# Kernel optimization log

Measured on AMD Instinct MI355X. Metric: run time of the kernel, lower is better.

Reference implementation:

```python
import jax, jax.numpy as jnp
import numpy as np

K = 3  # spline order
G = 5  # grid_size

def bspline(x):
    # Cox-de Boor B-spline basis over uniform grid on [-1,1] extended by K knots each side.
    h = 2.0 / G
    grid = jnp.arange(-K, G + K + 1, dtype=x.dtype) * h - 1.0  # [G+2K+1]
    xe = x[..., None]
    b = ((xe >= grid[:-1]) & (xe < grid[1:])).astype(x.dtype)  # order-0 bases [..., G+2K]
    for p in range(1, K + 1):
        b = ((xe - grid[:-(p + 1)]) / (grid[p:-1] - grid[:-(p + 1)]) * b[..., :-1]
             + (grid[p + 1:] - xe) / (grid[p + 1:] - grid[1:-p]) * b[..., 1:])
    return b  # [..., G+K]

def kan_conv(x, wb, ws, k):
    # x: [B,Cin,H,W] -> patches [B, Cin*k*k, H', W'] -> KANLinear per spatial position
    p = jax.lax.conv_general_dilated_patches(x, (k, k), (1, 1), 'VALID')
    p = jnp.moveaxis(p, 1, -1)  # [B,H',W',F]
    base = jax.nn.silu(p) @ wb.T
    spline = jnp.einsum('bhwig,oig->bhwo', bspline(p), ws)
    return jnp.moveaxis(base + spline, -1, 1)  # [B,Cout,H',W']

def maxpool2(x):
    return jax.lax.reduce_window(x, -jnp.inf, jax.lax.max, (1, 1, 2, 2), (1, 1, 2, 2), 'VALID')

def setup_inputs() -> dict:
    key = jax.random.key(0)
    ks = jax.random.split(key, 9)
    B = 4096
    s = 0.1
    return {
        'x': jax.random.normal(ks[0], (B, 1, 28, 28), jnp.float32),
        'wb1': jax.random.normal(ks[1], (5, 9), jnp.float32) * s,
        'ws1': jax.random.normal(ks[2], (5, 9, G + K), jnp.float32) * s,
        'wb2': jax.random.normal(ks[3], (5, 125), jnp.float32) * s,
        'ws2': jax.random.normal(ks[4], (5, 125, G + K), jnp.float32) * s,
        'wb3': jax.random.normal(ks[5], (2, 45), jnp.float32) * s,
        'ws3': jax.random.normal(ks[6], (2, 45, G + K), jnp.float32) * s,
        'fc_w': jax.random.normal(ks[7], (200, 98), jnp.float32) * s,
        'fc_b': jnp.zeros((200,), jnp.float32),
    }

def reference(x, wb1, ws1, wb2, ws2, wb3, ws3, fc_w, fc_b):
    h = kan_conv(x, wb1, ws1, 3)    # [B,5,26,26]
    h = maxpool2(h)                 # [B,5,13,13]
    h = kan_conv(h, wb2, ws2, 5)    # [B,5,9,9]
    h = kan_conv(h, wb3, ws3, 3)    # [B,2,7,7]
    h = h.reshape(h.shape[0], -1)   # [B,98]
    return h @ fc_w.T + fc_b        # [B,200]
```

## Files before the change

kernel.cpp:

```cpp
#include <hip/hip_runtime.h>


typedef _Float16 h2 __attribute__((ext_vector_type(2)));
typedef _Float16 f16x8 __attribute__((ext_vector_type(8)));
typedef float f32x4 __attribute__((ext_vector_type(4)));
typedef unsigned int uint_t;
typedef unsigned long long u64;

__device__ __forceinline__ uint_t pk(float a, float b) {
    h2 v; v[0] = (_Float16)a; v[1] = (_Float16)b;
    union { h2 h; uint_t u; } c; c.h = v; return c.u;
}

__device__ __forceinline__ float silu_f(float v) {
    return v / (1.0f + __expf(-v));
}

struct RecW { u64 R0, R1; uint_t R2; };
__device__ __forceinline__ RecW rec_words(float v) {
    float s  = silu_f(v);
    float t  = (v + 2.2f) * 2.5f;
    float cf = floorf(t);
    int   c  = (int)cf;
    float u  = t - cf;
    float u2 = u * u, u3 = u2 * u;
    float w  = 1.0f - u;
    const float k6 = 0.16666667f;
    float n0 = k6 * u3;
    float n1 = k6 * (-3.0f * u3 + 3.0f * u2 + 3.0f * u + 1.0f);
    float n2 = k6 * (3.0f * u3 - 6.0f * u2 + 4.0f);
    float n3 = k6 * (w * w * w);
    u64 H = ((u64)pk(n1, n0) << 32) | (u64)pk(n3, n2);
    if ((unsigned)c > 10u) H = 0;
    int cc = c < 0 ? 0 : (c > 10 ? 10 : c);
    int L  = cc * 16 - 48;
    u64 sl_lo = (L < 64) ? (H << (L & 63)) : 0;
    u64 hi_a  = (L == 0) ? 0 : (H >> ((64 - L) & 63));
    u64 hi_b  = H << ((L - 64) & 63);
    u64 sl_hi = (L < 64) ? hi_a : hi_b;
    u64 sr    = H >> ((-L) & 63);
    u64 B0 = (L >= 0) ? sl_lo : sr;
    u64 B1 = (L >= 0) ? sl_hi : 0;
    RecW r;
    r.R0 = (B0 << 16) | (u64)pk(s, 0.0f);
    r.R1 = (B0 >> 48) | (B1 << 16);
    r.R2 = (uint_t)(B1 >> 48);
    return r;
}

__device__ __forceinline__ void write_rec16s(_Float16* p, int off, float v) {
    RecW rw = rec_words(v);
    uint4 lo, hi;
    lo.x = (uint_t)rw.R0; lo.y = (uint_t)(rw.R0 >> 32);
    lo.z = (uint_t)rw.R1; lo.w = (uint_t)(rw.R1 >> 32);
    hi.x = rw.R2; hi.y = 0; hi.z = 0; hi.w = 0;
    *(uint4*)(p + off)       = lo;
    *(uint4*)(p + (8 ^ off)) = hi;
}

__device__ __forceinline__ void write_rec10(_Float16* p, float v) {
    RecW rw = rec_words(v);
    uint_t* d = (uint_t*)p;
    d[0] = (uint_t)rw.R0; d[1] = (uint_t)(rw.R0 >> 32);
    d[2] = (uint_t)rw.R1; d[3] = (uint_t)(rw.R1 >> 32);
    d[4] = rw.R2;
}

#define FCWT_BYTE_OFF   0
#define W1COL_BYTE_OFF  78400
#define W2COL_BYTE_OFF  80320
#define W3COL_BYTE_OFF  99520

__global__ __launch_bounds__(256) void kan_prep(
    const float* __restrict__ wb1, const float* __restrict__ ws1,
    const float* __restrict__ wb2, const float* __restrict__ ws2,
    const float* __restrict__ wb3, const float* __restrict__ ws3,
    const float* __restrict__ fcw, float* __restrict__ fcwT,
    _Float16* __restrict__ w1col, _Float16* __restrict__ w2col,
    _Float16* __restrict__ w3col)
{
    int gtid = blockIdx.x * 256 + threadIdx.x;
    int gstr = gridDim.x * 256;
    for (int i = gtid; i < 19600; i += gstr) {
        int o = i / 98, j = i % 98;
        fcwT[j * 200 + o] = fcw[i];
    }
    for (int i = gtid; i < 960; i += gstr) {
        int n = i / 160, k = i % 160;
        int rec = k >> 4, f = k & 15;
        float v = 0.f;
        if (n < 5 && rec < 9 && f < 9)
            v = (f == 0) ? wb1[n * 9 + rec] : ws1[(n * 9 + rec) * 8 + (f - 1)];
        w1col[i] = (_Float16)v;
    }
    for (int i = gtid; i < 9600; i += gstr) {
        int n = i / 1600, k2 = i % 1600;
        int tap = k2 >> 6, k = k2 & 63;
        int di = tap / 5, dj = tap % 5;
        int c = k / 10, f = k % 10;
        float v = 0.f;
        if (n < 5 && k < 50 && f < 9) {
            int r = n * 125 + c * 25 + di * 5 + dj;
            v = (f == 0) ? wb2[r] : ws2[r * 8 + (f - 1)];
        }
        w2col[i] = (_Float16)v;
    }
    for (int i = gtid; i < 3456; i += gstr) {
        int n = i / 576, k2 = i % 576;
        int tap = k2 >> 6, k = k2 & 63;
        int di = tap / 3, dj = tap % 3;
        int c = k / 10, f = k % 10;
        float v = 0.f;
        if (n < 2 && k < 50 && f < 9) {
            int r = n * 45 + c * 9 + di * 3 + dj;
            v = (f == 0) ? wb3[r] : ws3[r * 8 + (f - 1)];
        }
        w3col[i] = (_Float16)v;
    }
}

__global__ __launch_bounds__(256) void kan_fused(
    const float* __restrict__ x,
    const _Float16* __restrict__ w1col,
    const _Float16* __restrict__ w2col,
    const _Float16* __restrict__ w3col,
    const float* __restrict__ fcwT,
    const float* __restrict__ fcb,
    float* __restrict__ out)
{
    __shared__ __align__(16) _Float16 smemA[12544];
    __shared__ __align__(16) float    smemB[504];
    float* buf = smemB;
    float* h3f = smemB + 405;

    const int b   = blockIdx.x;
    const int tid = threadIdx.x;
    const int wv  = __builtin_amdgcn_readfirstlane(tid >> 6);
    const int ln  = tid & 63;

    const int m   = ln & 15;
    const int kb  = ln >> 4;
    const int hr  = kb >> 1;
    const int s8  = (kb & 1) * 8;
    const int nn  = m < 5 ? m : 5;

#pragma unroll 1
    for (int i = tid; i < 784; i += 256)
        write_rec16s(&smemA[i * 16], (i & 4) << 1, x[b * 784 + i]);
    __syncthreads();

    {
        f16x8 Bf[5];
#pragma unroll
        for (int ks = 0; ks < 5; ++ks)
            Bf[ks] = *(const f16x8*)(w1col + nn * 160 + ks * 32 + kb * 8);
        const int dpix[10] = {0, 1, 2, 28, 29, 30, 56, 57, 58, 0};
#pragma unroll 1
        for (int tile = wv; tile < 43; tile += 4) {
            int p = tile * 16 + m; p = p > 675 ? 675 : p;
            int pix0 = (p / 26) * 28 + (p % 26);
            f32x4 acc = {0.f, 0.f, 0.f, 0.f};
#pragma unroll
            for (int ks = 0; ks < 5; ++ks) {
                int dp = hr ? dpix[2 * ks + 1] : dpix[2 * ks];
                int p2 = pix0 + dp;
                int addr = p2 * 16 + (s8 ^ ((p2 & 4) << 1));
                f16x8 av = *(const f16x8*)(smemA + addr);
                acc = __builtin_amdgcn_mfma_f32_16x16x32_f16(av, Bf[ks], acc, 0, 0, 0);
            }
            int srow = tile * 16 + kb * 4;
#pragma unroll
            for (int r = 0; r < 4; ++r) {
                int s = srow + r;
                if (m < 5 && s < 676)
                    smemA[s * 16 + (8 ^ ((s & 4) << 1)) + 2 + m] = (_Float16)acc[r];
            }
        }
    }
    __syncthreads();

    float mx0, mx1, mx2, mx3 = 0.f;
    {
        auto pool = [&](int i) -> float {
            int pp = i / 5, c = i % 5;
            int ph = pp / 13, pw = pp % 13;
            int s0 = ph * 52 + pw * 2;
            int s1 = s0 + 1, s2 = s0 + 26, s3 = s0 + 27;
            float v00 = (float)smemA[s0 * 16 + (8 ^ ((s0 & 4) << 1)) + 2 + c];
            float v01 = (float)smemA[s1 * 16 + (8 ^ ((s1 & 4) << 1)) + 2 + c];
            float v10 = (float)smemA[s2 * 16 + (8 ^ ((s2 & 4) << 1)) + 2 + c];
            float v11 = (float)smemA[s3 * 16 + (8 ^ ((s3 & 4) << 1)) + 2 + c];
            return fmaxf(fmaxf(v00, v01), fmaxf(v10, v11));
        };
        mx0 = pool(tid);
        mx1 = pool(tid + 256);
        mx2 = pool(tid + 512);
        if (tid < 77) mx3 = pool(tid + 768);
    }
    __syncthreads();

    {
        auto st = [&](int i, float v) {
            int pp = i / 5, c = i % 5;
            write_rec10(&smemA[pp * 72 + c * 10], v);
        };
        st(tid, mx0);
        st(tid + 256, mx1);
        st(tid + 512, mx2);
        if (tid < 77) st(tid + 768, mx3);
    }
    __syncthreads();

    {
        int p0 = wv * 16 + m;       p0 = p0 > 80 ? 80 : p0;
        int p1 = (wv + 4) * 16 + m; p1 = p1 > 80 ? 80 : p1;
        int ry0 = (p0 / 9) * 13 + (p0 % 9);
        int ry1 = (p1 / 9) * 13 + (p1 % 9);
        const bool two = (wv < 2);
        f32x4 acc0 = {0.f, 0.f, 0.f, 0.f}, acc1 = {0.f, 0.f, 0.f, 0.f};
#pragma unroll 1
        for (int tap = 0; tap < 25; ++tap) {
            int di = tap / 5, dj = tap % 5;
            const _Float16* wrow = w2col + nn * 1600 + tap * 64 + kb * 8;
            f16x8 bv0 = *(const f16x8*)(wrow);
            f16x8 bv1 = *(const f16x8*)(wrow + 32);
            int qoff = di * 13 + dj;
            const _Float16* ab0 = smemA + (ry0 + qoff) * 72 + kb * 8;
            acc0 = __builtin_amdgcn_mfma_f32_16x16x32_f16(*(const f16x8*)(ab0),      bv0, acc0, 0, 0, 0);
            acc0 = __builtin_amdgcn_mfma_f32_16x16x32_f16(*(const f16x8*)(ab0 + 32), bv1, acc0, 0, 0, 0);
            if (two) {
                const _Float16* ab1 = smemA + (ry1 + qoff) * 72 + kb * 8;
                acc1 = __builtin_amdgcn_mfma_f32_16x16x32_f16(*(const f16x8*)(ab1),      bv0, acc1, 0, 0, 0);
                acc1 = __builtin_amdgcn_mfma_f32_16x16x32_f16(*(const f16x8*)(ab1 + 32), bv1, acc1, 0, 0, 0);
            }
        }
        int prow = kb * 4;
#pragma unroll
        for (int r = 0; r < 4; ++r) {
            int pp0 = wv * 16 + prow + r;
            if (m < 5 && pp0 < 81) buf[m * 81 + pp0] = acc0[r];
            int pp1 = (wv + 4) * 16 + prow + r;
            if (two && m < 5 && pp1 < 81) buf[m * 81 + pp1] = acc1[r];
        }
    }
    __syncthreads();

#pragma unroll 1
    for (int i = tid; i < 405; i += 256) {
        int pp = i / 5, o = i % 5;
        write_rec10(&smemA[pp * 72 + o * 10], buf[o * 81 + pp]);
    }
    __syncthreads();

    {
        int p3 = wv * 16 + m; p3 = p3 > 48 ? 48 : p3;
        int ry3 = (p3 / 7) * 9 + (p3 % 7);
        f32x4 acc = {0.f, 0.f, 0.f, 0.f};
#pragma unroll 1
        for (int tap = 0; tap < 9; ++tap) {
            int di = tap / 3, dj = tap % 3;
            const _Float16* wrow = w3col + nn * 576 + tap * 64 + kb * 8;
            f16x8 bv0 = *(const f16x8*)(wrow);
            f16x8 bv1 = *(const f16x8*)(wrow + 32);
            const _Float16* ab = smemA + (ry3 + di * 9 + dj) * 72 + kb * 8;
            acc = __builtin_amdgcn_mfma_f32_16x16x32_f16(*(const f16x8*)(ab),      bv0, acc, 0, 0, 0);
            acc = __builtin_amdgcn_mfma_f32_16x16x32_f16(*(const f16x8*)(ab + 32), bv1, acc, 0, 0, 0);
        }
#pragma unroll
        for (int r = 0; r < 4; ++r) {
            int pout = wv * 16 + kb * 4 + r;
            if (m < 2 && pout < 49) h3f[m * 49 + pout] = acc[r];
        }
    }
    __syncthreads();

    if (tid < 200) {
        float a0 = 0.f, a1 = 0.f;
#pragma unroll 7
        for (int j = 0; j < 98; j += 2) {
            a0 += fcwT[j * 200 + tid]       * h3f[j];
            a1 += fcwT[(j + 1) * 200 + tid] * h3f[j + 1];
        }
        out[b * 200 + tid] = fcb[tid] + a0 + a1;
    }
}

extern "C" void kernel_launch(void* const* d_in, const int* in_sizes, int n_in,
                              void* d_out, int out_size, void* d_ws, size_t ws_size,
                              hipStream_t stream) {
    const float* x   = (const float*)d_in[0];
    const float* wb1 = (const float*)d_in[1];
    const float* ws1 = (const float*)d_in[2];
    const float* wb2 = (const float*)d_in[3];
    const float* ws2 = (const float*)d_in[4];
    const float* wb3 = (const float*)d_in[5];
    const float* ws3 = (const float*)d_in[6];
    const float* fcw = (const float*)d_in[7];
    const float* fcb = (const float*)d_in[8];
    float* out = (float*)d_out;

    float*    fcwT  = (float*)((char*)d_ws + FCWT_BYTE_OFF);
    _Float16* w1col = (_Float16*)((char*)d_ws + W1COL_BYTE_OFF);
    _Float16* w2col = (_Float16*)((char*)d_ws + W2COL_BYTE_OFF);
    _Float16* w3col = (_Float16*)((char*)d_ws + W3COL_BYTE_OFF);

    kan_prep<<<32, 256, 0, stream>>>(wb1, ws1, wb2, ws2, wb3, ws3, fcw,
                                     fcwT, w1col, w2col, w3col);

    int B = in_sizes[0] / 784;
    kan_fused<<<B, 256, 0, stream>>>(x, w1col, w2col, w3col, fcwT, fcb, out);
}
```

Measured before the change: 169.8 us.

## Split conv2 MFMA work across waves by tap with LDS atomic reduction

Conv2 was split over waves by output-pixel tile, so waves 0-1 did two tiles and waves 2-3 did one, which left the load uneven. Each wave now takes a strided subset of the 25 taps across all 6 pixel tiles. The partial sums are combined with shared-memory atomicAdd into a buffer that is zeroed at kernel start. This evens out MFMA work per wave, but adds 24 float atomics per lane, an extra zeroing pass, and more accumulator registers. The h3f buffer now aliases buf to save LDS.

```diff
diff --git a/kernel.cpp b/kernel.cpp
--- a/kernel.cpp
+++ b/kernel.cpp
@@ -129,9 +129,9 @@
     float* __restrict__ out)
 {
     __shared__ __align__(16) _Float16 smemA[12544];
-    __shared__ __align__(16) float    smemB[504];
+    __shared__ __align__(16) float    smemB[408];
     float* buf = smemB;
-    float* h3f = smemB + 405;
+    float* h3f = smemB;
 
     const int b   = blockIdx.x;
     const int tid = threadIdx.x;
@@ -144,6 +144,8 @@
     const int s8  = (kb & 1) * 8;
     const int nn  = m < 5 ? m : 5;
 
+#pragma unroll
+    for (int i = tid; i < 408; i += 256) smemB[i] = 0.f;
 #pragma unroll 1
     for (int i = tid; i < 784; i += 256)
         write_rec16s(&smemA[i * 16], (i & 4) << 1, x[b * 784 + i]);
@@ -212,35 +214,39 @@
     __syncthreads();
 
     {
-        int p0 = wv * 16 + m;       p0 = p0 > 80 ? 80 : p0;
-        int p1 = (wv + 4) * 16 + m; p1 = p1 > 80 ? 80 : p1;
-        int ry0 = (p0 / 9) * 13 + (p0 % 9);
-        int ry1 = (p1 / 9) * 13 + (p1 % 9);
-        const bool two = (wv < 2);
-        f32x4 acc0 = {0.f, 0.f, 0.f, 0.f}, acc1 = {0.f, 0.f, 0.f, 0.f};
-#pragma unroll 1
-        for (int tap = 0; tap < 25; ++tap) {
+        int ryb[6];
+#pragma unroll
+        for (int t = 0; t < 6; ++t) {
+            int p = t * 16 + m; p = p > 80 ? 80 : p;
+            ryb[t] = (p / 9) * 13 + (p % 9);
+        }
+        f32x4 acc[6];
+#pragma unroll
+        for (int t = 0; t < 6; ++t) { f32x4 z = {0.f,0.f,0.f,0.f}; acc[t] = z; }
+#pragma unroll 1
+        for (int tap = wv; tap < 25; tap += 4) {
             int di = tap / 5, dj = tap % 5;
             const _Float16* wrow = w2col + nn * 1600 + tap * 64 + kb * 8;
             f16x8 bv0 = *(const f16x8*)(wrow);
             f16x8 bv1 = *(const f16x8*)(wrow + 32);
             int qoff = di * 13 + dj;
-            const _Float16* ab0 = smemA + (ry0 + qoff) * 72 + kb * 8;
-            acc0 = __builtin_amdgcn_mfma_f32_16x16x32_f16(*(const f16x8*)(ab0),      bv0, acc0, 0, 0, 0);
-            acc0 = __builtin_amdgcn_mfma_f32_16x16x32_f16(*(const f16x8*)(ab0 + 32), bv1, acc0, 0, 0, 0);
-            if (two) {
-                const _Float16* ab1 = smemA + (ry1 + qoff) * 72 + kb * 8;
-                acc1 = __builtin_amdgcn_mfma_f32_16x16x32_f16(*(const f16x8*)(ab1),      bv0, acc1, 0, 0, 0);
-                acc1 = __builtin_amdgcn_mfma_f32_16x16x32_f16(*(const f16x8*)(ab1 + 32), bv1, acc1, 0, 0, 0);
+#pragma unroll
+            for (int t = 0; t < 6; ++t) {
+                const _Float16* ab = smemA + (ryb[t] + qoff) * 72 + kb * 8;
+                acc[t] = __builtin_amdgcn_mfma_f32_16x16x32_f16(
+                             *(const f16x8*)(ab), bv0, acc[t], 0, 0, 0);
+                acc[t] = __builtin_amdgcn_mfma_f32_16x16x32_f16(
+                             *(const f16x8*)(ab + 32), bv1, acc[t], 0, 0, 0);
             }
         }
         int prow = kb * 4;
 #pragma unroll
-        for (int r = 0; r < 4; ++r) {
-            int pp0 = wv * 16 + prow + r;
-            if (m < 5 && pp0 < 81) buf[m * 81 + pp0] = acc0[r];
-            int pp1 = (wv + 4) * 16 + prow + r;
-            if (two && m < 5 && pp1 < 81) buf[m * 81 + pp1] = acc1[r];
+        for (int t = 0; t < 6; ++t) {
+#pragma unroll
+            for (int r = 0; r < 4; ++r) {
+                int pp = t * 16 + prow + r;
+                if (m < 5 && pp < 81) atomicAdd(&buf[m * 81 + pp], acc[t][r]);
+            }
         }
     }
     __syncthreads();
```

New measurement: 172.9 us. About the same (+1.8%).
